# Optimization experiments

Measured on AMD Instinct MI355X. Metric: run time of the kernel, lower is better.

## Reference

```python
import jax, jax.numpy as jnp
import numpy as np

MASK_OUT_VALUE = -10000.0


def setup_inputs() -> dict:
    key = jax.random.key(0)
    k1, k2, k3 = jax.random.split(key, 3)
    B, H, S, D = 2, 16, 2048, 64
    query = jax.random.normal(k1, (B, H, S, D), dtype=jnp.float32)
    key_t = jax.random.normal(k2, (B, H, S, D), dtype=jnp.float32)
    value = jax.random.normal(k3, (B, H, S, D), dtype=jnp.float32)
    # causal mask: (1, 1, S, S), True where attention is allowed
    mask = jnp.tril(jnp.ones((S, S), dtype=bool))[None, None, :, :]
    return {"query": query, "key": key_t, "value": value, "mask": mask}


def reference(query, key, value, mask):
    # scores: (B, H, S, S)
    scale = 1.0 / jnp.sqrt(jnp.asarray(query.shape[-1], query.dtype))
    attn_scores = jnp.einsum("bhqd,bhkd->bhqk", query, key) * scale
    attn_scores = jnp.where(mask, attn_scores,
                            jnp.asarray(MASK_OUT_VALUE, attn_scores.dtype))
    attn_weights = jax.nn.softmax(attn_scores, axis=-1)
    # dropout is identity (p=0 / eval mode)
    attn_output = jnp.einsum("bhqk,bhkd->bhqd", attn_weights, value)
    return attn_output
```

## Files before the change

### kernel.cpp

```cpp
#include <hip/hip_runtime.h>
#include <math.h>


#define S_LEN   2048
#define D_HEAD  64
#define SCALE_L2E 0.18033688011112042f
#define FIXM    8.0f

using bf16x8 = __attribute__((ext_vector_type(8))) short;
using f32x4  = __attribute__((ext_vector_type(4))) float;

__device__ __forceinline__ unsigned int rnd_bf(float f) {
  return __float_as_uint(f) + 0x8000u;
}
__device__ __forceinline__ unsigned short f2bf(float f) {
  return (unsigned short)(rnd_bf(f) >> 16);
}

__device__ __forceinline__ void gl_lds16(const unsigned short* g, unsigned short* l) {
  __builtin_amdgcn_global_load_lds(
      (const __attribute__((address_space(1))) unsigned int*)g,
      (__attribute__((address_space(3))) unsigned int*)l, 16, 0, 0);
}

template <int CTRL>
__device__ __forceinline__ float dppf(float x) {
  return __builtin_bit_cast(float,
      __builtin_amdgcn_update_dpp(0, __builtin_bit_cast(int, x), CTRL, 0xF, 0xF, false));
}
__device__ __forceinline__ float rowsum16(float x) {
  x += dppf<0xB1>(x);
  x += dppf<0x4E>(x);
  x += dppf<0x124>(x);
  x += dppf<0x128>(x);
  return x;
}

__global__ __launch_bounds__(256, 4)
void prep(const float* __restrict__ Kg, const float* __restrict__ Vg,
          unsigned short* __restrict__ Kb, unsigned short* __restrict__ Vt)
{
  __shared__ __align__(16) unsigned short Lt[64][72];
  const int j = blockIdx.x, t = threadIdx.x;
  const int bh = j >> 4, seg = j & 15;
  const size_t base = (size_t)bh * (S_LEN * D_HEAD) + (size_t)seg * 128 * D_HEAD;
#pragma unroll
  for (int i = 0; i < 8; ++i) {
    const size_t idx = base + i * 1024 + t * 4;
    const f32x4 v = *(const f32x4*)(Kg + idx);
    uint2 pk;
    pk.x = (rnd_bf(v[1]) & 0xFFFF0000u) | (rnd_bf(v[0]) >> 16);
    pk.y = (rnd_bf(v[3]) & 0xFFFF0000u) | (rnd_bf(v[2]) >> 16);
    *(uint2*)(Kb + idx) = pk;
  }
  for (int h = 0; h < 2; ++h) {
    const int s0 = seg * 128 + h * 64;
    __syncthreads();
#pragma unroll
    for (int pp = 0; pp < 4; ++pp) {
      const int r = t >> 2;
      const int d0 = (t & 3) * 4 + pp * 16;
      const f32x4 v = *(const f32x4*)(Vg + (size_t)bh * (S_LEN * D_HEAD)
                                         + (size_t)(s0 + r) * D_HEAD + d0);
#pragma unroll
      for (int e = 0; e < 4; ++e) Lt[d0 + e][r] = f2bf(v[e]);
    }
    __syncthreads();
#pragma unroll
    for (int q = 0; q < 2; ++q) {
      const int d = t >> 2, ch = (t & 3) + 4 * q;
      *(uint4*)(Vt + (size_t)(bh * 64 + d) * S_LEN + s0 + ch * 8) =
          *(const uint4*)&Lt[d][ch * 8];
    }
  }
}

__global__ __launch_bounds__(256, 4)
void fa(const float* __restrict__ Qg, const unsigned short* __restrict__ Kb,
        const unsigned short* __restrict__ Vt, float* __restrict__ Og)
{
  __shared__ unsigned short Ks[2][64][64];
  __shared__ unsigned short Vs[2][64][64];
  __shared__ unsigned short Ps[4][16][64];

  const int id = blockIdx.x;
  const int bh = id & 31;
  const int p  = id >> 5;

  const int t    = threadIdx.x;
  const int w    = t >> 6;
  const int lane = t & 63;
  const int c    = lane & 15;
  const int quad = lane >> 4;

  const float* __restrict__ Qb = Qg + (size_t)bh * (S_LEN * D_HEAD);
  float* __restrict__ Ob = Og + (size_t)bh * (S_LEN * D_HEAD);

  const int wv   = w & 1;
  const int row0 = (w >= 2) ? (S_LEN - 32 * (p + 1) + 16 * wv)
                            : (32 * p + 16 * wv);
  const int ktdiag = row0 >> 6;
  const int ktmax  = (S_LEN - 1 - 32 * p) >> 6;

  bf16x8 qa[2];
  {
    const float* qp = Qb + (size_t)(row0 + c) * D_HEAD + quad * 8;
#pragma unroll
    for (int h = 0; h < 2; ++h) {
      f32x4 a0 = *(const f32x4*)(qp + 32 * h);
      f32x4 a1 = *(const f32x4*)(qp + 32 * h + 4);
#pragma unroll
      for (int j = 0; j < 4; ++j) {
        qa[h][j]     = (short)f2bf(a0[j] * SCALE_L2E);
        qa[h][4 + j] = (short)f2bf(a1[j] * SCALE_L2E);
      }
    }
  }

  int fOff[4][2];
#pragma unroll
  for (int ci = 0; ci < 4; ++ci)
#pragma unroll
    for (int h = 0; h < 2; ++h)
      fOff[ci][h] = ((ci * 16 + c) << 6) + (((h * 4 + quad) ^ (c & 7)) << 3);
  int pw[4][4];
#pragma unroll
  for (int ci = 0; ci < 4; ++ci)
#pragma unroll
    for (int r = 0; r < 4; ++r) {
      const int prow = quad * 4 + r, pcol = ci * 16 + c;
      pw[ci][r] = (prow << 6) + ((((pcol >> 3) ^ (prow & 7)) << 3) | (pcol & 7));
    }
  int prd[2];
#pragma unroll
  for (int h = 0; h < 2; ++h)
    prd[h] = (c << 6) + (((h * 4 + quad) ^ (c & 7)) << 3);

  f32x4 oa[4];
  float ls[4];
#pragma unroll
  for (int i = 0; i < 4; ++i) {
    oa[i] = (f32x4){0.f, 0.f, 0.f, 0.f};
    ls[i] = 0.f;
  }

  const int rl = lane >> 3;
  const int jj = (lane & 7) ^ rl;
  auto stage = [&](int kt, int buf) {
#pragma unroll
    for (int n = 0; n < 2; ++n) {
      const int row = w * 16 + n * 8 + rl;
      gl_lds16(Kb + (((size_t)(bh * S_LEN + kt * 64 + row)) << 6) + jj * 8,
               &Ks[buf][w * 16 + n * 8][0]);
      gl_lds16(Vt + (((size_t)(bh * 64 + row)) << 11) + kt * 64 + jj * 8,
               &Vs[buf][w * 16 + n * 8][0]);
    }
  };

  stage(0, 0);
  for (int kt = 0; kt <= ktmax; ++kt) {
    const int cur = kt & 1;
    __syncthreads();
    if (kt < ktmax) stage(kt + 1, cur ^ 1);

    if (kt <= ktdiag) {
      const unsigned short* ksc = &Ks[cur][0][0];
      const unsigned short* vsc = &Vs[cur][0][0];
      bf16x8 kf[4][2], vf[4][2];
#pragma unroll
      for (int ci = 0; ci < 4; ++ci)
#pragma unroll
        for (int h = 0; h < 2; ++h) {
          kf[ci][h] = *(const bf16x8*)(ksc + fOff[ci][h]);
          vf[ci][h] = *(const bf16x8*)(vsc + fOff[ci][h]);
        }

      f32x4 sc[4];
#pragma unroll
      for (int ci = 0; ci < 4; ++ci) {
        f32x4 acc = (f32x4){-FIXM, -FIXM, -FIXM, -FIXM};
        acc = __builtin_amdgcn_mfma_f32_16x16x32_bf16(qa[0], kf[ci][0], acc, 0, 0, 0);
        acc = __builtin_amdgcn_mfma_f32_16x16x32_bf16(qa[1], kf[ci][1], acc, 0, 0, 0);
        sc[ci] = acc;
      }
      if (kt == ktdiag) {
#pragma unroll
        for (int ci = 0; ci < 4; ++ci) {
          const int gcol = kt * 64 + ci * 16 + c;
#pragma unroll
          for (int r = 0; r < 4; ++r)
            if (gcol > row0 + quad * 4 + r) sc[ci][r] = -1e30f;
        }
      }
#pragma unroll
      for (int ci = 0; ci < 4; ++ci)
#pragma unroll
        for (int r = 0; r < 4; ++r)
          sc[ci][r] = __builtin_amdgcn_exp2f(sc[ci][r]);
#pragma unroll
      for (int r = 0; r < 4; ++r)
        ls[r] += (sc[0][r] + sc[1][r]) + (sc[2][r] + sc[3][r]);
      unsigned short* psw = &Ps[w][0][0];
#pragma unroll
      for (int ci = 0; ci < 4; ++ci)
#pragma unroll
        for (int r = 0; r < 4; ++r)
          psw[pw[ci][r]] = f2bf(sc[ci][r]);
      const bf16x8 pa0 = *(const bf16x8*)(psw + prd[0]);
      const bf16x8 pa1 = *(const bf16x8*)(psw + prd[1]);
#pragma unroll
      for (int ci = 0; ci < 4; ++ci) {
        oa[ci] = __builtin_amdgcn_mfma_f32_16x16x32_bf16(pa0, vf[ci][0], oa[ci], 0, 0, 0);
        oa[ci] = __builtin_amdgcn_mfma_f32_16x16x32_bf16(pa1, vf[ci][1], oa[ci], 0, 0, 0);
      }
    }
  }

  {
    float inv[4];
#pragma unroll
    for (int r = 0; r < 4; ++r) inv[r] = 1.0f / rowsum16(ls[r]);
#pragma unroll
    for (int ci = 0; ci < 4; ++ci)
#pragma unroll
      for (int r = 0; r < 4; ++r)
        Ob[(size_t)(row0 + quad * 4 + r) * D_HEAD + ci * 16 + c] = oa[ci][r] * inv[r];
  }
}

__global__ __launch_bounds__(256, 4)
void fa_fb(const float* __restrict__ Qg, const float* __restrict__ Kg,
           const float* __restrict__ Vg, float* __restrict__ Og)
{
  __shared__ __align__(16) unsigned short Ksh[64][72];
  __shared__ __align__(16) unsigned short Vsh[64][72];
  __shared__ __align__(16) unsigned short Psh[4][16][72];
  const int id = blockIdx.x;
  const int bh = id & 31;
  const int p  = id >> 5;
  const int t    = threadIdx.x;
  const int w    = t >> 6;
  const int lane = t & 63;
  const int c    = lane & 15;
  const int quad = lane >> 4;
  const size_t base = (size_t)bh * (S_LEN * D_HEAD);
  const float* __restrict__ Qb = Qg + base;
  const float* __restrict__ Kb = Kg + base;
  const float* __restrict__ Vb = Vg + base;
  float* __restrict__ Ob = Og + base;
  const int wv   = w & 1;
  const int row0 = (w >= 2) ? (S_LEN - 32 * (p + 1) + 16 * wv) : (32 * p + 16 * wv);
  const int ktdiag = row0 >> 6;
  const int ktmax  = (S_LEN - 1 - 32 * p) >> 6;
  bf16x8 qa[2];
  {
    const float* qp = Qb + (size_t)(row0 + c) * D_HEAD + quad * 8;
#pragma unroll
    for (int h = 0; h < 2; ++h) {
      f32x4 a0 = *(const f32x4*)(qp + 32 * h);
      f32x4 a1 = *(const f32x4*)(qp + 32 * h + 4);
#pragma unroll
      for (int j = 0; j < 4; ++j) {
        qa[h][j]     = (short)f2bf(a0[j] * SCALE_L2E);
        qa[h][4 + j] = (short)f2bf(a1[j] * SCALE_L2E);
      }
    }
  }
  f32x4 oa[4];
  float ls[4];
#pragma unroll
  for (int i = 0; i < 4; ++i) {
    oa[i] = (f32x4){0.f, 0.f, 0.f, 0.f};
    ls[i] = 0.f;
  }
  for (int kt = 0; kt <= ktmax; ++kt) {
    __syncthreads();
    {
      const int cp = t & 15;
      const int rg = t >> 4;
      const int col0 = cp * 4;
      const int sw = (cp >> 2) << 3;
#pragma unroll
      for (int i = 0; i < 4; ++i) {
        const int row = i * 16 + rg;
        const size_t goff = (size_t)(kt * 64 + row) * D_HEAD + col0;
        const f32x4 kv = *(const f32x4*)(Kb + goff);
        const f32x4 vv = *(const f32x4*)(Vb + goff);
        const unsigned int k01 = (rnd_bf(kv[1]) & 0xFFFF0000u) | (rnd_bf(kv[0]) >> 16);
        const unsigned int k23 = (rnd_bf(kv[3]) & 0xFFFF0000u) | (rnd_bf(kv[2]) >> 16);
        *(uint2*)&Ksh[row][col0] = make_uint2(k01, k23);
        const int kz = row ^ sw;
#pragma unroll
        for (int e = 0; e < 4; ++e)
          Vsh[col0 + e][kz] = f2bf(vv[e]);
      }
    }
    __syncthreads();
    if (kt <= ktdiag) {
      bf16x8 kf[4][2], vf[4][2];
#pragma unroll
      for (int ci = 0; ci < 4; ++ci) {
        kf[ci][0] = *(const bf16x8*)&Ksh[ci * 16 + c][quad * 8];
        kf[ci][1] = *(const bf16x8*)&Ksh[ci * 16 + c][32 + quad * 8];
        vf[ci][0] = *(const bf16x8*)&Vsh[ci * 16 + c][(quad ^ ci) * 8];
        vf[ci][1] = *(const bf16x8*)&Vsh[ci * 16 + c][32 + ((quad ^ ci) * 8)];
      }
      f32x4 sc[4];
#pragma unroll
      for (int ci = 0; ci < 4; ++ci) {
        f32x4 acc = (f32x4){-FIXM, -FIXM, -FIXM, -FIXM};
        acc = __builtin_amdgcn_mfma_f32_16x16x32_bf16(qa[0], kf[ci][0], acc, 0, 0, 0);
        acc = __builtin_amdgcn_mfma_f32_16x16x32_bf16(qa[1], kf[ci][1], acc, 0, 0, 0);
        sc[ci] = acc;
      }
      if (kt == ktdiag) {
#pragma unroll
        for (int ci = 0; ci < 4; ++ci) {
          const int gcol = kt * 64 + ci * 16 + c;
#pragma unroll
          for (int r = 0; r < 4; ++r)
            if (gcol > row0 + quad * 4 + r) sc[ci][r] = -1e30f;
        }
      }
#pragma unroll
      for (int ci = 0; ci < 4; ++ci)
#pragma unroll
        for (int r = 0; r < 4; ++r)
          sc[ci][r] = __builtin_amdgcn_exp2f(sc[ci][r]);
#pragma unroll
      for (int r = 0; r < 4; ++r)
        ls[r] += (sc[0][r] + sc[1][r]) + (sc[2][r] + sc[3][r]);
#pragma unroll
      for (int ci = 0; ci < 4; ++ci)
#pragma unroll
        for (int r = 0; r < 4; ++r) {
          const int prow = quad * 4 + r;
          Psh[w][prow][(ci * 16 + c) ^ ((prow >> 3) << 3)] = f2bf(sc[ci][r]);
        }
      const int px = (c >> 3) << 3;
      const bf16x8 pa0 = *(const bf16x8*)&Psh[w][c][(quad * 8) ^ px];
      const bf16x8 pa1 = *(const bf16x8*)&Psh[w][c][((32 + quad * 8)) ^ px];
#pragma unroll
      for (int ci = 0; ci < 4; ++ci) {
        oa[ci] = __builtin_amdgcn_mfma_f32_16x16x32_bf16(pa0, vf[ci][0], oa[ci], 0, 0, 0);
        oa[ci] = __builtin_amdgcn_mfma_f32_16x16x32_bf16(pa1, vf[ci][1], oa[ci], 0, 0, 0);
      }
    }
  }
  {
    float inv[4];
#pragma unroll
    for (int r = 0; r < 4; ++r) inv[r] = 1.0f / rowsum16(ls[r]);
#pragma unroll
    for (int ci = 0; ci < 4; ++ci)
#pragma unroll
      for (int r = 0; r < 4; ++r)
        Ob[(size_t)(row0 + quad * 4 + r) * D_HEAD + ci * 16 + c] = oa[ci][r] * inv[r];
  }
}

extern "C" void kernel_launch(void* const* d_in, const int* in_sizes, int n_in,
                              void* d_out, int out_size, void* d_ws, size_t ws_size,
                              hipStream_t stream) {
  (void)in_sizes; (void)n_in; (void)out_size;
  const float* Q = (const float*)d_in[0];
  const float* K = (const float*)d_in[1];
  const float* V = (const float*)d_in[2];
  float* O = (float*)d_out;
  const size_t NEED = 2ull * 32 * S_LEN * D_HEAD * 2;
  if (ws_size >= NEED) {
    unsigned short* Kb = (unsigned short*)d_ws;
    unsigned short* Vt = Kb + (size_t)32 * S_LEN * D_HEAD;
    prep<<<dim3(512), dim3(256), 0, stream>>>(K, V, Kb, Vt);
    fa<<<dim3(1024), dim3(256), 0, stream>>>(Q, Kb, Vt, O);
  } else {
    fa_fb<<<dim3(1024), dim3(256), 0, stream>>>(Q, K, V, O);
  }
}
```

Baseline: 139.2 us.

## Compute transposed scores to keep P in registers and double rows per wave

```diff
diff --git a/kernel.cpp b/kernel.cpp
--- a/kernel.cpp
+++ b/kernel.cpp
@@ -8,7 +8,11 @@
 #define FIXM    8.0f
 
 using bf16x8 = __attribute__((ext_vector_type(8))) short;
+using bf16x4 = __attribute__((ext_vector_type(4))) short;
 using f32x4  = __attribute__((ext_vector_type(4))) float;
+
+#define MFMA32(A,B,C) __builtin_amdgcn_mfma_f32_16x16x32_bf16((A),(B),(C),0,0,0)
+#define MFMA16(A,B,C) __builtin_amdgcn_mfma_f32_16x16x16bf16_1k((A),(B),(C),0,0,0)
 
 __device__ __forceinline__ unsigned int rnd_bf(float f) {
   return __float_as_uint(f) + 0x8000u;
@@ -75,13 +79,13 @@
   }
 }
 
-__global__ __launch_bounds__(256, 4)
+__global__ __launch_bounds__(256, 2)
 void fa(const float* __restrict__ Qg, const unsigned short* __restrict__ Kb,
         const unsigned short* __restrict__ Vt, float* __restrict__ Og)
 {
   __shared__ unsigned short Ks[2][64][64];
   __shared__ unsigned short Vs[2][64][64];
-  __shared__ unsigned short Ps[4][16][64];
+  __shared__ __align__(16) float Lred[4][2][4][16];
 
   const int id = blockIdx.x;
   const int bh = id & 31;
@@ -96,23 +100,23 @@
   const float* __restrict__ Qb = Qg + (size_t)bh * (S_LEN * D_HEAD);
   float* __restrict__ Ob = Og + (size_t)bh * (S_LEN * D_HEAD);
 
-  const int wv   = w & 1;
-  const int row0 = (w >= 2) ? (S_LEN - 32 * (p + 1) + 16 * wv)
-                            : (32 * p + 16 * wv);
-  const int ktdiag = row0 >> 6;
-  const int ktmax  = (S_LEN - 1 - 32 * p) >> 6;
-
-  bf16x8 qa[2];
-  {
-    const float* qp = Qb + (size_t)(row0 + c) * D_HEAD + quad * 8;
+  const int rw = (w < 2) ? (64 * p + 32 * w)
+                         : (S_LEN - 64 * (p + 1) + 32 * (w - 2));
+  const int ktdiag = rw >> 6;
+  const int ktmax  = 31 - p;
+
+  bf16x8 qb[2][2];
+#pragma unroll
+  for (int rt = 0; rt < 2; ++rt) {
+    const float* qp = Qb + (size_t)(rw + 16 * rt + c) * D_HEAD + quad * 8;
 #pragma unroll
     for (int h = 0; h < 2; ++h) {
       f32x4 a0 = *(const f32x4*)(qp + 32 * h);
       f32x4 a1 = *(const f32x4*)(qp + 32 * h + 4);
 #pragma unroll
       for (int j = 0; j < 4; ++j) {
-        qa[h][j]     = (short)f2bf(a0[j] * SCALE_L2E);
-        qa[h][4 + j] = (short)f2bf(a1[j] * SCALE_L2E);
+        qb[rt][h][j]     = (short)f2bf(a0[j] * SCALE_L2E);
+        qb[rt][h][4 + j] = (short)f2bf(a1[j] * SCALE_L2E);
       }
     }
   }
@@ -123,26 +127,22 @@
 #pragma unroll
     for (int h = 0; h < 2; ++h)
       fOff[ci][h] = ((ci * 16 + c) << 6) + (((h * 4 + quad) ^ (c & 7)) << 3);
-  int pw[4][4];
-#pragma unroll
-  for (int ci = 0; ci < 4; ++ci)
-#pragma unroll
-    for (int r = 0; r < 4; ++r) {
-      const int prow = quad * 4 + r, pcol = ci * 16 + c;
-      pw[ci][r] = (prow << 6) + ((((pcol >> 3) ^ (prow & 7)) << 3) | (pcol & 7));
-    }
-  int prd[2];
-#pragma unroll
-  for (int h = 0; h < 2; ++h)
-    prd[h] = (c << 6) + (((h * 4 + quad) ^ (c & 7)) << 3);
-
-  f32x4 oa[4];
-  float ls[4];
-#pragma unroll
-  for (int i = 0; i < 4; ++i) {
-    oa[i] = (f32x4){0.f, 0.f, 0.f, 0.f};
-    ls[i] = 0.f;
-  }
+  int vOff[4][4];
+#pragma unroll
+  for (int ks = 0; ks < 4; ++ks)
+#pragma unroll
+    for (int cid = 0; cid < 4; ++cid)
+      vOff[ks][cid] = ((cid * 16 + c) << 6)
+                    + (((ks * 2 + (quad >> 1)) ^ (c & 7)) << 3)
+                    + ((quad & 1) << 2);
+
+  f32x4 oa[2][4];
+  float ls[2] = {0.f, 0.f};
+#pragma unroll
+  for (int rt = 0; rt < 2; ++rt)
+#pragma unroll
+    for (int i = 0; i < 4; ++i)
+      oa[rt][i] = (f32x4){0.f, 0.f, 0.f, 0.f};
 
   const int rl = lane >> 3;
   const int jj = (lane & 7) ^ rl;
@@ -166,66 +166,86 @@
     if (kt <= ktdiag) {
       const unsigned short* ksc = &Ks[cur][0][0];
       const unsigned short* vsc = &Vs[cur][0][0];
-      bf16x8 kf[4][2], vf[4][2];
+      bf16x8 kf[4][2];
 #pragma unroll
       for (int ci = 0; ci < 4; ++ci)
 #pragma unroll
-        for (int h = 0; h < 2; ++h) {
+        for (int h = 0; h < 2; ++h)
           kf[ci][h] = *(const bf16x8*)(ksc + fOff[ci][h]);
-          vf[ci][h] = *(const bf16x8*)(vsc + fOff[ci][h]);
-        }
-
-      f32x4 sc[4];
-#pragma unroll
-      for (int ci = 0; ci < 4; ++ci) {
-        f32x4 acc = (f32x4){-FIXM, -FIXM, -FIXM, -FIXM};
-        acc = __builtin_amdgcn_mfma_f32_16x16x32_bf16(qa[0], kf[ci][0], acc, 0, 0, 0);
-        acc = __builtin_amdgcn_mfma_f32_16x16x32_bf16(qa[1], kf[ci][1], acc, 0, 0, 0);
-        sc[ci] = acc;
-      }
-      if (kt == ktdiag) {
+      bf16x4 vf[4][4];
+#pragma unroll
+      for (int ks = 0; ks < 4; ++ks)
+#pragma unroll
+        for (int cid = 0; cid < 4; ++cid)
+          vf[ks][cid] = *(const bf16x4*)(vsc + vOff[ks][cid]);
+
+#pragma unroll
+      for (int rt = 0; rt < 2; ++rt) {
+        f32x4 st[4];
 #pragma unroll
         for (int ci = 0; ci < 4; ++ci) {
-          const int gcol = kt * 64 + ci * 16 + c;
+          f32x4 acc = (f32x4){-FIXM, -FIXM, -FIXM, -FIXM};
+          acc = MFMA32(kf[ci][0], qb[rt][0], acc);
+          acc = MFMA32(kf[ci][1], qb[rt][1], acc);
+          st[ci] = acc;
+        }
+        if (kt == ktdiag) {
+          const int qrow = rw + 16 * rt + c;
+#pragma unroll
+          for (int ci = 0; ci < 4; ++ci) {
+            const int kbase = kt * 64 + ci * 16 + quad * 4;
+#pragma unroll
+            for (int r = 0; r < 4; ++r)
+              if (kbase + r > qrow) st[ci][r] = -1e30f;
+          }
+        }
+#pragma unroll
+        for (int ci = 0; ci < 4; ++ci)
 #pragma unroll
           for (int r = 0; r < 4; ++r)
-            if (gcol > row0 + quad * 4 + r) sc[ci][r] = -1e30f;
-        }
-      }
-#pragma unroll
-      for (int ci = 0; ci < 4; ++ci)
-#pragma unroll
-        for (int r = 0; r < 4; ++r)
-          sc[ci][r] = __builtin_amdgcn_exp2f(sc[ci][r]);
+            st[ci][r] = __builtin_amdgcn_exp2f(st[ci][r]);
+        ls[rt] += ((st[0][0] + st[0][1] + st[0][2] + st[0][3])
+                 + (st[1][0] + st[1][1] + st[1][2] + st[1][3]))
+                + ((st[2][0] + st[2][1] + st[2][2] + st[2][3])
+                 + (st[3][0] + st[3][1] + st[3][2] + st[3][3]));
+        bf16x4 pa[4];
+#pragma unroll
+        for (int ci = 0; ci < 4; ++ci)
+          pa[ci] = (bf16x4){(short)f2bf(st[ci][0]), (short)f2bf(st[ci][1]),
+                            (short)f2bf(st[ci][2]), (short)f2bf(st[ci][3])};
+#pragma unroll
+        for (int cid = 0; cid < 4; ++cid) {
+          f32x4 o = oa[rt][cid];
+          o = MFMA16(pa[0], vf[0][cid], o);
+          o = MFMA16(pa[1], vf[1][cid], o);
+          o = MFMA16(pa[2], vf[2][cid], o);
+          o = MFMA16(pa[3], vf[3][cid], o);
+          oa[rt][cid] = o;
+        }
+      }
+    }
+  }
+
+  Lred[w][0][quad][c] = ls[0];
+  Lred[w][1][quad][c] = ls[1];
+  float inv[2][4];
+#pragma unroll
+  for (int rt = 0; rt < 2; ++rt) {
+    f32x4 s = (f32x4){0.f, 0.f, 0.f, 0.f};
+#pragma unroll
+    for (int q = 0; q < 4; ++q)
+      s += *(const f32x4*)&Lred[w][rt][q][quad * 4];
+#pragma unroll
+    for (int r = 0; r < 4; ++r) inv[rt][r] = 1.0f / s[r];
+  }
+#pragma unroll
+  for (int rt = 0; rt < 2; ++rt)
+#pragma unroll
+    for (int cid = 0; cid < 4; ++cid)
 #pragma unroll
       for (int r = 0; r < 4; ++r)
-        ls[r] += (sc[0][r] + sc[1][r]) + (sc[2][r] + sc[3][r]);
-      unsigned short* psw = &Ps[w][0][0];
-#pragma unroll
-      for (int ci = 0; ci < 4; ++ci)
-#pragma unroll
-        for (int r = 0; r < 4; ++r)
-          psw[pw[ci][r]] = f2bf(sc[ci][r]);
-      const bf16x8 pa0 = *(const bf16x8*)(psw + prd[0]);
-      const bf16x8 pa1 = *(const bf16x8*)(psw + prd[1]);
-#pragma unroll
-      for (int ci = 0; ci < 4; ++ci) {
-        oa[ci] = __builtin_amdgcn_mfma_f32_16x16x32_bf16(pa0, vf[ci][0], oa[ci], 0, 0, 0);
-        oa[ci] = __builtin_amdgcn_mfma_f32_16x16x32_bf16(pa1, vf[ci][1], oa[ci], 0, 0, 0);
-      }
-    }
-  }
-
-  {
-    float inv[4];
-#pragma unroll
-    for (int r = 0; r < 4; ++r) inv[r] = 1.0f / rowsum16(ls[r]);
-#pragma unroll
-    for (int ci = 0; ci < 4; ++ci)
-#pragma unroll
-      for (int r = 0; r < 4; ++r)
-        Ob[(size_t)(row0 + quad * 4 + r) * D_HEAD + ci * 16 + c] = oa[ci][r] * inv[r];
-  }
+        Ob[(size_t)(rw + 16 * rt + quad * 4 + r) * D_HEAD + cid * 16 + c] =
+            oa[rt][cid][r] * inv[rt][r];
 }
 
 __global__ __launch_bounds__(256, 4)
@@ -309,8 +329,8 @@
 #pragma unroll
       for (int ci = 0; ci < 4; ++ci) {
         f32x4 acc = (f32x4){-FIXM, -FIXM, -FIXM, -FIXM};
-        acc = __builtin_amdgcn_mfma_f32_16x16x32_bf16(qa[0], kf[ci][0], acc, 0, 0, 0);
-        acc = __builtin_amdgcn_mfma_f32_16x16x32_bf16(qa[1], kf[ci][1], acc, 0, 0, 0);
+        acc = MFMA32(qa[0], kf[ci][0], acc);
+        acc = MFMA32(qa[1], kf[ci][1], acc);
         sc[ci] = acc;
       }
       if (kt == ktdiag) {
@@ -342,8 +362,8 @@
       const bf16x8 pa1 = *(const bf16x8*)&Psh[w][c][((32 + quad * 8)) ^ px];
 #pragma unroll
       for (int ci = 0; ci < 4; ++ci) {
-        oa[ci] = __builtin_amdgcn_mfma_f32_16x16x32_bf16(pa0, vf[ci][0], oa[ci], 0, 0, 0);
-        oa[ci] = __builtin_amdgcn_mfma_f32_16x16x32_bf16(pa1, vf[ci][1], oa[ci], 0, 0, 0);
+        oa[ci] = MFMA32(pa0, vf[ci][0], oa[ci]);
+        oa[ci] = MFMA32(pa1, vf[ci][1], oa[ci]);
       }
     }
   }
@@ -372,7 +392,7 @@
     unsigned short* Kb = (unsigned short*)d_ws;
     unsigned short* Vt = Kb + (size_t)32 * S_LEN * D_HEAD;
     prep<<<dim3(512), dim3(256), 0, stream>>>(K, V, Kb, Vt);
-    fa<<<dim3(1024), dim3(256), 0, stream>>>(Q, Kb, Vt, O);
+    fa<<<dim3(512), dim3(256), 0, stream>>>(Q, Kb, Vt, O);
   } else {
     fa_fb<<<dim3(1024), dim3(256), 0, stream>>>(Q, K, V, O);
   }
```

Result: slower. 145.1 us (+4.2%).
